# Kernel optimization log

Measured on AMD Instinct MI355X. Metric: run time of the kernel, lower is better.

## Reference

```python
import jax, jax.numpy as jnp
import numpy as np

EPS = 1e-12  # matches F.normalize default eps

def _l2_normalize(x, axis=-1):
    n = jnp.sqrt(jnp.sum(x * x, axis=axis, keepdims=True))
    return x / jnp.maximum(n, EPS)

def setup_inputs() -> dict:
    key = jax.random.key(0)
    k1, k2, k3 = jax.random.split(key, 3)
    B, C, D, V = 1024, 262144, 512, 512
    query = jax.random.normal(k1, (B, D), dtype=jnp.float32)
    keys = jax.random.normal(k2, (C, D), dtype=jnp.float32)
    values = jax.random.normal(k3, (C, V), dtype=jnp.float32)
    return {"query": query, "keys": keys, "values": values, "k": 8}

def reference(query, keys, values, k):
    # Cosine similarity: normalize both sides, then GEMM.
    q_norm = _l2_normalize(query, axis=1)          # [B, D]
    k_norm = _l2_normalize(keys, axis=1)           # [C, D]
    scores = jnp.matmul(q_norm, k_norm.T)          # [B, C]
    top_scores, top_indices = jax.lax.top_k(scores, k)  # [B, k] each
    # Vectorized gather replacing the per-row Python loop:
    retrieved_values = values[top_indices]         # [B, k, V]
    return retrieved_values, top_scores, top_indices
```

## Files before the change

kernel.cpp:

```cpp
#include <hip/hip_runtime.h>
#include <hip/hip_bf16.h>
#include <stdint.h>

#define B_Q   1024
#define C_K   262144
#define D_DIM 512
#define V_DIM 512
#define K_TOP 8
#define BM 128
#define BN 128
#define BK 64
#define NT (C_K/BN)
#define MT (B_Q/BM)
#define NKT (D_DIM/BK)
#define TPB 32
#define CAP 2048
#define QS 8.0f
#define TAU_S 8.64f
#define RWIN 64
#define SC1 0x7F7F7F7F

typedef float f32x4  __attribute__((ext_vector_type(4)));
typedef float f32x16 __attribute__((ext_vector_type(16)));
typedef int   i32x8  __attribute__((ext_vector_type(8)));
typedef __attribute__((address_space(3))) unsigned char lds_uchar;
typedef __attribute__((address_space(1))) const unsigned char gbl_uchar;

__global__ __launch_bounds__(256) void nrm_rows(const float* __restrict__ in,
                                                uint8_t* __restrict__ out,
                                                int nrows, int* cnt, int ncnt){
  if (cnt != nullptr && blockIdx.x == 0){
    for (int i = threadIdx.x; i < ncnt; i += 256) cnt[i] = 0;
  }
  int row  = blockIdx.x*4 + (threadIdx.x>>6);
  int lane = threadIdx.x & 63;
  if (row >= nrows) return;
  const float4* r4 = (const float4*)(in + (size_t)row*D_DIM);
  float4 a = r4[lane*2], b = r4[lane*2+1];
  float ss = a.x*a.x+a.y*a.y+a.z*a.z+a.w*a.w
           + b.x*b.x+b.y*b.y+b.z*b.z+b.w*b.w;
  #pragma unroll
  for (int off=32; off>0; off>>=1) ss += __shfl_xor(ss, off);
  float rn = QS / fmaxf(sqrtf(ss), 1e-12f);
  int w0 = __builtin_amdgcn_cvt_pk_fp8_f32(a.x*rn, a.y*rn, 0,  false);
  w0     = __builtin_amdgcn_cvt_pk_fp8_f32(a.z*rn, a.w*rn, w0, true);
  int w1 = __builtin_amdgcn_cvt_pk_fp8_f32(b.x*rn, b.y*rn, 0,  false);
  w1     = __builtin_amdgcn_cvt_pk_fp8_f32(b.z*rn, b.w*rn, w1, true);
  ((uint2*)(out + (size_t)row*D_DIM))[lane] = make_uint2((unsigned)w0, (unsigned)w1);
}

__global__ __launch_bounds__(512, 4) void gemm_topk(const uint8_t* __restrict__ qn,
                                                    const uint8_t* __restrict__ kn,
                                                    int* __restrict__ cnt,
                                                    float2* __restrict__ cand){
  extern __shared__ __align__(16) unsigned char smem[];

  const int tid  = threadIdx.x;
  const int lane = tid & 63;
  const int w    = tid >> 6;
  const int wm = w >> 2, wn = w & 3;

  const unsigned bid = blockIdx.x;
  const int xcd  = bid & 7;
  const int s    = bid >> 3;
  const int mt   = s & 7;
  const int nt0  = xcd*256 + (s >> 3)*TPB;

  f32x16 acc0 = {0}, acc1 = {0};

  const uint8_t* ab  = qn + (size_t)mt*BM*D_DIM;
  const uint8_t* bb0 = kn + (size_t)nt0*BN*D_DIM;

  const int srow = tid >> 2;
  const unsigned ssw = (unsigned)(((tid & 3) ^ ((srow >> 1) & 3)) << 4);
  const uint8_t* aptr = ab  + (size_t)srow*D_DIM + ssw;
  const uint8_t* bptr = bb0 + (size_t)srow*D_DIM + ssw;
  const unsigned dst0 = (unsigned)tid*16u;

  #define STAGE_KT(buf_) do{                                                    \
    const unsigned cb_ = (unsigned)(buf_)*16384u;                                \
    __builtin_amdgcn_global_load_lds((gbl_uchar*)(aptr),                         \
        (lds_uchar*)(smem + cb_ + dst0), 16, 0, 0);                              \
    __builtin_amdgcn_global_load_lds((gbl_uchar*)(bptr),                         \
        (lds_uchar*)(smem + cb_ + 8192u + dst0), 16, 0, 0);                      \
  }while(0)

  #define UOFF(row_, u_) \
    ((unsigned)((row_)*64 + (((u_) ^ (((row_)>>1)&3))<<4)))

  union frag8 { uint4 q[2]; i32x8 v; };

  STAGE_KT(0);
  aptr += 64; bptr += 64;
  __syncthreads();

  const int kh2 = (lane >> 5) * 2;
  const int rA0 = wm*64 + (lane & 31);
  const int rA1 = rA0 + 32;
  const int rB  = wn*32 + (lane & 31);

  for (int kt=0; kt<TPB*NKT; kt++){
    const unsigned cbase = (unsigned)(kt&1)*16384u;

    if (kt < TPB*NKT-1){
      STAGE_KT((kt+1)&1);
      const bool wrap = ((kt+1)&7) == 7;
      aptr += wrap ? -(7*64) : 64;
      bptr += wrap ? ((size_t)BN*D_DIM - 7*64) : 64;
      asm volatile("s_waitcnt vmcnt(2)" ::: "memory");
    } else {
      asm volatile("s_waitcnt vmcnt(0)" ::: "memory");
    }
    __builtin_amdgcn_sched_barrier(0);
    __builtin_amdgcn_s_barrier();

    frag8 fa0, fa1, fb;
    fa0.q[0] = *(const uint4*)(smem + cbase + UOFF(rA0, kh2));
    fa0.q[1] = *(const uint4*)(smem + cbase + UOFF(rA0, kh2+1));
    fb.q[0]  = *(const uint4*)(smem + cbase + 8192u + UOFF(rB, kh2));
    fb.q[1]  = *(const uint4*)(smem + cbase + 8192u + UOFF(rB, kh2+1));
    fa1.q[0] = *(const uint4*)(smem + cbase + UOFF(rA1, kh2));
    fa1.q[1] = *(const uint4*)(smem + cbase + UOFF(rA1, kh2+1));
    __builtin_amdgcn_s_setprio(1);
    acc0 = __builtin_amdgcn_mfma_scale_f32_32x32x64_f8f6f4(
               fa0.v, fb.v, acc0, 0, 0, 0, SC1, 0, SC1);
    acc1 = __builtin_amdgcn_mfma_scale_f32_32x32x64_f8f6f4(
               fa1.v, fb.v, acc1, 0, 0, 0, SC1, 0, SC1);
    __builtin_amdgcn_s_setprio(0);
    asm volatile("s_waitcnt lgkmcnt(0)" ::: "memory");
    __builtin_amdgcn_sched_barrier(0);
    __builtin_amdgcn_s_barrier();

    if ((kt & (NKT-1)) == NKT-1){
      const int ntc  = nt0 + (kt >> 3);
      const int colg = ntc*BN + wn*32 + (lane&31);
      #pragma unroll
      for (int mh=0; mh<2; mh++){
        f32x16 a = mh ? acc1 : acc0;
        const int rbase = mt*BM + wm*64 + mh*32 + 4*(lane>>5);
        #pragma unroll
        for (int qd=0; qd<4; qd++){
          float v0=a[qd*4+0], v1=a[qd*4+1], v2=a[qd*4+2], v3=a[qd*4+3];
          float mx = fmaxf(fmaxf(v0,v1), fmaxf(v2,v3));
          if (mx > TAU_S){
            #pragma unroll
            for (int jj=0; jj<4; jj++){
              float v = a[qd*4+jj];
              if (v > TAU_S){
                int rowg = rbase + jj + 8*qd;
                int pos = atomicAdd(cnt + rowg, 1);
                if (pos < CAP)
                  cand[(size_t)rowg*CAP + pos] = make_float2(v, __int_as_float(colg));
              }
            }
          }
        }
      }
      acc0 = (f32x16){0}; acc1 = (f32x16){0};
    }
  }
  #undef STAGE_KT
  #undef UOFF
}

__global__ __launch_bounds__(256) void merge_rescore(const int* __restrict__ cnt,
                                                     const float2* __restrict__ cand,
                                                     const float* __restrict__ q,
                                                     const float* __restrict__ keys,
                                                     const float* __restrict__ values,
                                                     float* __restrict__ out){
  const int qi = blockIdx.x, tid = threadIdx.x;
  const int lane = tid & 63, w = tid >> 6;
  __shared__ __align__(16) float qrow[D_DIM];
  __shared__ __align__(16) float2 ent[CAP];
  __shared__ int    widx[RWIN];
  __shared__ double dsc[RWIN];
  __shared__ double wq[4];
  __shared__ int    fidx[8];
  __shared__ double fsc[8];

  float2 qv = ((const float2*)(q + (size_t)qi*D_DIM))[tid];
  qrow[tid*2] = qv.x; qrow[tid*2+1] = qv.y;
  double pq = (double)qv.x*qv.x + (double)qv.y*qv.y;
  #pragma unroll
  for (int off=32; off>0; off>>=1) pq += __shfl_xor(pq, off);
  if (lane == 0) wq[w] = pq;

  const int n = min(cnt[qi], CAP);
  for (int i = tid; i < n; i += 256) ent[i] = cand[(size_t)qi*CAP + i];
  if (tid < RWIN) widx[tid] = -1;
  __syncthreads();
  double qq = wq[0]+wq[1]+wq[2]+wq[3];

  for (int e = tid; e < n; e += 256){
    float se = ent[e].x; int ce = __float_as_int(ent[e].y);
    int rank = 0;
    for (int jx = 0; jx < n; jx++){
      float sj = ent[jx].x; int cj = __float_as_int(ent[jx].y);
      rank += (sj > se) || (sj == se && cj < ce);
    }
    if (rank < RWIN) widx[rank] = ce;
  }
  __syncthreads();

  const int g = tid >> 2, sub = tid & 3;
  const int ki = widx[g];
  const int kis = (ki < 0) ? 0 : ki;
  const float4* kr4 = (const float4*)(keys + (size_t)kis*D_DIM);
  const float4* qr4 = (const float4*)qrow;
  double da = 0.0, dk = 0.0;
  for (int i=0;i<32;i++){
    float4 kv  = kr4[sub*32+i];
    float4 qv4 = qr4[sub*32+i];
    da += (double)qv4.x*kv.x + (double)qv4.y*kv.y + (double)qv4.z*kv.z + (double)qv4.w*kv.w;
    dk += (double)kv.x*kv.x + (double)kv.y*kv.y + (double)kv.z*kv.z + (double)kv.w*kv.w;
  }
  da += __shfl_down(da, 2, 4); da += __shfl_down(da, 1, 4);
  dk += __shfl_down(dk, 2, 4); dk += __shfl_down(dk, 1, 4);
  if (sub == 0){
    double nq = fmax(sqrt(qq), 1e-12);
    double nk = fmax(sqrt(dk), 1e-12);
    dsc[g] = (ki < 0) ? -1e300 : da/(nq*nk);
  }
  __syncthreads();

  if (tid == 0){
    for (int s=0; s<8; s++){
      double bs = -1e301; int bi = 0; int bx = 0x7fffffff;
      for (int c=0; c<RWIN; c++){
        double v = dsc[c]; int ix = widx[c];
        if (v > bs || (v == bs && ix >= 0 && ix < bx)){ bs = v; bi = c; bx = ix; }
      }
      fsc[s] = bs; fidx[s] = (bx == 0x7fffffff) ? 0 : bx;
      dsc[bi] = -1e302;
    }
  }
  __syncthreads();

  float* out_sc  = out + (size_t)B_Q*K_TOP*V_DIM;
  float* out_idx = out_sc + (size_t)B_Q*K_TOP;
  if (tid < 8){
    out_sc [qi*K_TOP + tid] = (float)fsc[tid];
    out_idx[qi*K_TOP + tid] = (float)fidx[tid];
  }
  #pragma unroll
  for (int s=0; s<8; s++){
    const float2* vr = (const float2*)(values + (size_t)fidx[s]*V_DIM);
    float2* orow = (float2*)(out + ((size_t)qi*K_TOP + s)*V_DIM);
    orow[tid] = vr[tid];
  }
}

extern "C" void kernel_launch(void* const* d_in, const int* in_sizes, int n_in,
                              void* d_out, int out_size, void* d_ws, size_t ws_size,
                              hipStream_t stream){
  const float* q      = (const float*)d_in[0];
  const float* keys   = (const float*)d_in[1];
  const float* values = (const float*)d_in[2];
  unsigned char* ws = (unsigned char*)d_ws;
  uint8_t* qn = (uint8_t*)ws;
  uint8_t* kn = qn + (size_t)B_Q*D_DIM;
  int*    cnt  = (int*)(ws + (size_t)(B_Q + C_K)*D_DIM);
  float2* cand = (float2*)(ws + (size_t)(B_Q + C_K)*D_DIM + 8192);
  float* out = (float*)d_out;

  hipFuncSetAttribute((const void*)gemm_topk,
                      hipFuncAttributeMaxDynamicSharedMemorySize, 65536);

  nrm_rows<<<dim3(B_Q/4), dim3(256), 0, stream>>>(q, qn, B_Q, cnt, B_Q);
  nrm_rows<<<dim3(C_K/4), dim3(256), 0, stream>>>(keys, kn, C_K, nullptr, 0);
  gemm_topk<<<dim3(512), dim3(512), 32768, stream>>>(qn, kn, cnt, cand);
  merge_rescore<<<dim3(B_Q), dim3(256), 0, stream>>>(cnt, cand, q, keys, values, out);
}
```

Before: 461.9 us.

## Pre-pack FP8 rows in MFMA fragment order, keep Q tile in LDS, stream keys via registers

The normalize kernel now writes FP8 rows in a 32-row-tile, MFMA-fragment-ordered layout. The GEMM loads the whole 128x512 query tile into LDS once (64KB dynamic LDS) and streams key fragments straight from global memory into registers with a one-step software prefetch. This removes per-k-step LDS staging, the swizzle arithmetic and two barriers per iteration. In exchange, each key fragment is read by every wave directly from global/L2 with no sharing through LDS, and the larger LDS footprint may lower occupancy.

```diff
diff --git a/kernel.cpp b/kernel.cpp
--- a/kernel.cpp
+++ b/kernel.cpp
@@ -9,10 +9,8 @@
 #define K_TOP 8
 #define BM 128
 #define BN 128
-#define BK 64
 #define NT (C_K/BN)
-#define MT (B_Q/BM)
-#define NKT (D_DIM/BK)
+#define NKT 8
 #define TPB 32
 #define CAP 2048
 #define QS 8.0f
@@ -26,9 +24,9 @@
 typedef __attribute__((address_space(3))) unsigned char lds_uchar;
 typedef __attribute__((address_space(1))) const unsigned char gbl_uchar;
 
-__global__ __launch_bounds__(256) void nrm_rows(const float* __restrict__ in,
-                                                uint8_t* __restrict__ out,
-                                                int nrows, int* cnt, int ncnt){
+__global__ __launch_bounds__(256) void pack_rows(const float* __restrict__ in,
+                                                 uint8_t* __restrict__ outp,
+                                                 int nrows, int* cnt, int ncnt){
   if (cnt != nullptr && blockIdx.x == 0){
     for (int i = threadIdx.x; i < ncnt; i += 256) cnt[i] = 0;
   }
@@ -46,14 +44,19 @@
   w0     = __builtin_amdgcn_cvt_pk_fp8_f32(a.z*rn, a.w*rn, w0, true);
   int w1 = __builtin_amdgcn_cvt_pk_fp8_f32(b.x*rn, b.y*rn, 0,  false);
   w1     = __builtin_amdgcn_cvt_pk_fp8_f32(b.z*rn, b.w*rn, w1, true);
-  ((uint2*)(out + (size_t)row*D_DIM))[lane] = make_uint2((unsigned)w0, (unsigned)w1);
-}
-
-__global__ __launch_bounds__(512, 4) void gemm_topk(const uint8_t* __restrict__ qn,
-                                                    const uint8_t* __restrict__ kn,
+  const int j  = lane;
+  const int rt = row >> 5, rr = row & 31;
+  const int kt = j >> 3, h = (j >> 2) & 1, sub = (j >> 1) & 1;
+  uint2* dst = (uint2*)(outp + ((size_t)(rt*8 + kt))*2048
+                        + sub*1024 + (rr + 32*h)*16 + (j & 1)*8);
+  *dst = make_uint2((unsigned)w0, (unsigned)w1);
+}
+
+__global__ __launch_bounds__(512, 4) void gemm_topk(const uint8_t* __restrict__ qp,
+                                                    const uint8_t* __restrict__ kp,
                                                     int* __restrict__ cnt,
                                                     float2* __restrict__ cand){
-  extern __shared__ __align__(16) unsigned char smem[];
+  extern __shared__ __align__(16) unsigned char alds[];
 
   const int tid  = threadIdx.x;
   const int lane = tid & 63;
@@ -66,73 +69,51 @@
   const int mt   = s & 7;
   const int nt0  = xcd*256 + (s >> 3)*TPB;
 
+  #pragma unroll
+  for (int i=0; i<8; i++)
+    __builtin_amdgcn_global_load_lds(
+        (gbl_uchar*)(qp + (size_t)mt*65536u + tid*16 + i*8192),
+        (lds_uchar*)(alds + tid*16 + i*8192), 16, 0, 0);
+  __syncthreads();
+
   f32x16 acc0 = {0}, acc1 = {0};
-
-  const uint8_t* ab  = qn + (size_t)mt*BM*D_DIM;
-  const uint8_t* bb0 = kn + (size_t)nt0*BN*D_DIM;
-
-  const int srow = tid >> 2;
-  const unsigned ssw = (unsigned)(((tid & 3) ^ ((srow >> 1) & 3)) << 4);
-  const uint8_t* aptr = ab  + (size_t)srow*D_DIM + ssw;
-  const uint8_t* bptr = bb0 + (size_t)srow*D_DIM + ssw;
-  const unsigned dst0 = (unsigned)tid*16u;
-
-  #define STAGE_KT(buf_) do{                                                    \
-    const unsigned cb_ = (unsigned)(buf_)*16384u;                                \
-    __builtin_amdgcn_global_load_lds((gbl_uchar*)(aptr),                         \
-        (lds_uchar*)(smem + cb_ + dst0), 16, 0, 0);                              \
-    __builtin_amdgcn_global_load_lds((gbl_uchar*)(bptr),                         \
-        (lds_uchar*)(smem + cb_ + 8192u + dst0), 16, 0, 0);                      \
-  }while(0)
-
-  #define UOFF(row_, u_) \
-    ((unsigned)((row_)*64 + (((u_) ^ (((row_)>>1)&3))<<4)))
-
   union frag8 { uint4 q[2]; i32x8 v; };
 
-  STAGE_KT(0);
-  aptr += 64; bptr += 64;
-  __syncthreads();
-
-  const int kh2 = (lane >> 5) * 2;
-  const int rA0 = wm*64 + (lane & 31);
-  const int rA1 = rA0 + 32;
-  const int rB  = wn*32 + (lane & 31);
-
-  for (int kt=0; kt<TPB*NKT; kt++){
-    const unsigned cbase = (unsigned)(kt&1)*16384u;
-
-    if (kt < TPB*NKT-1){
-      STAGE_KT((kt+1)&1);
-      const bool wrap = ((kt+1)&7) == 7;
-      aptr += wrap ? -(7*64) : 64;
-      bptr += wrap ? ((size_t)BN*D_DIM - 7*64) : 64;
-      asm volatile("s_waitcnt vmcnt(2)" ::: "memory");
-    } else {
-      asm volatile("s_waitcnt vmcnt(0)" ::: "memory");
-    }
-    __builtin_amdgcn_sched_barrier(0);
-    __builtin_amdgcn_s_barrier();
-
-    frag8 fa0, fa1, fb;
-    fa0.q[0] = *(const uint4*)(smem + cbase + UOFF(rA0, kh2));
-    fa0.q[1] = *(const uint4*)(smem + cbase + UOFF(rA0, kh2+1));
-    fb.q[0]  = *(const uint4*)(smem + cbase + 8192u + UOFF(rB, kh2));
-    fb.q[1]  = *(const uint4*)(smem + cbase + 8192u + UOFF(rB, kh2+1));
-    fa1.q[0] = *(const uint4*)(smem + cbase + UOFF(rA1, kh2));
-    fa1.q[1] = *(const uint4*)(smem + cbase + UOFF(rA1, kh2+1));
-    __builtin_amdgcn_s_setprio(1);
-    acc0 = __builtin_amdgcn_mfma_scale_f32_32x32x64_f8f6f4(
-               fa0.v, fb.v, acc0, 0, 0, 0, SC1, 0, SC1);
-    acc1 = __builtin_amdgcn_mfma_scale_f32_32x32x64_f8f6f4(
-               fa1.v, fb.v, acc1, 0, 0, 0, SC1, 0, SC1);
-    __builtin_amdgcn_s_setprio(0);
-    asm volatile("s_waitcnt lgkmcnt(0)" ::: "memory");
-    __builtin_amdgcn_sched_barrier(0);
-    __builtin_amdgcn_s_barrier();
-
-    if ((kt & (NKT-1)) == NKT-1){
-      const int ntc  = nt0 + (kt >> 3);
+  const uint8_t* bptr = kp + ((size_t)(nt0*4 + wn)*8)*2048 + (unsigned)lane*16u;
+  uint4 pf0 = *(const uint4*)(bptr);
+  uint4 pf1 = *(const uint4*)(bptr + 1024);
+
+  const unsigned aoffA = (unsigned)(wm*16)*2048u + (unsigned)lane*16u;
+
+  for (int t=0; t<TPB; t++){
+    #pragma unroll
+    for (int k8=0; k8<8; k8++){
+      const bool last = (t == TPB-1) && (k8 == 7);
+      const uint8_t* bnext = bptr + (k8 == 7 ? 25*2048 : 2048);
+      uint4 nf0, nf1;
+      if (!last){
+        nf0 = *(const uint4*)(bnext);
+        nf1 = *(const uint4*)(bnext + 1024);
+      }
+      frag8 fa0, fa1, fb;
+      const unsigned ao = aoffA + (unsigned)k8*2048u;
+      fa0.q[0] = *(const uint4*)(alds + ao);
+      fa0.q[1] = *(const uint4*)(alds + ao + 1024u);
+      fa1.q[0] = *(const uint4*)(alds + ao + 16384u);
+      fa1.q[1] = *(const uint4*)(alds + ao + 16384u + 1024u);
+      fb.q[0] = pf0; fb.q[1] = pf1;
+      __builtin_amdgcn_s_setprio(1);
+      acc0 = __builtin_amdgcn_mfma_scale_f32_32x32x64_f8f6f4(
+                 fa0.v, fb.v, acc0, 0, 0, 0, SC1, 0, SC1);
+      acc1 = __builtin_amdgcn_mfma_scale_f32_32x32x64_f8f6f4(
+                 fa1.v, fb.v, acc1, 0, 0, 0, SC1, 0, SC1);
+      __builtin_amdgcn_s_setprio(0);
+      pf0 = nf0; pf1 = nf1;
+      bptr = bnext;
+    }
+
+    {
+      const int ntc  = nt0 + t;
       const int colg = ntc*BN + wn*32 + (lane&31);
       #pragma unroll
       for (int mh=0; mh<2; mh++){
@@ -159,8 +140,6 @@
       acc0 = (f32x16){0}; acc1 = (f32x16){0};
     }
   }
-  #undef STAGE_KT
-  #undef UOFF
 }
 
 __global__ __launch_bounds__(256) void merge_rescore(const int* __restrict__ cnt,
@@ -258,8 +237,8 @@
   const float* keys   = (const float*)d_in[1];
   const float* values = (const float*)d_in[2];
   unsigned char* ws = (unsigned char*)d_ws;
-  uint8_t* qn = (uint8_t*)ws;
-  uint8_t* kn = qn + (size_t)B_Q*D_DIM;
+  uint8_t* qp = (uint8_t*)ws;
+  uint8_t* kp = qp + (size_t)B_Q*D_DIM;
   int*    cnt  = (int*)(ws + (size_t)(B_Q + C_K)*D_DIM);
   float2* cand = (float2*)(ws + (size_t)(B_Q + C_K)*D_DIM + 8192);
   float* out = (float*)d_out;
@@ -267,8 +246,8 @@
   hipFuncSetAttribute((const void*)gemm_topk,
                       hipFuncAttributeMaxDynamicSharedMemorySize, 65536);
 
-  nrm_rows<<<dim3(B_Q/4), dim3(256), 0, stream>>>(q, qn, B_Q, cnt, B_Q);
-  nrm_rows<<<dim3(C_K/4), dim3(256), 0, stream>>>(keys, kn, C_K, nullptr, 0);
-  gemm_topk<<<dim3(512), dim3(512), 32768, stream>>>(qn, kn, cnt, cand);
+  pack_rows<<<dim3(B_Q/4), dim3(256), 0, stream>>>(q, qp, B_Q, cnt, B_Q);
+  pack_rows<<<dim3(C_K/4), dim3(256), 0, stream>>>(keys, kp, C_K, nullptr, 0);
+  gemm_topk<<<dim3(512), dim3(512), 65536, stream>>>(qp, kp, cnt, cand);
   merge_rescore<<<dim3(B_Q), dim3(256), 0, stream>>>(cnt, cand, q, keys, values, out);
 }
```

After: 963.4 us. 2.09x slower.
